# Kernel tuning notes

Measured on AMD Instinct MI355X. Metric: run time of the kernel, lower is better.

The kernel has to match this reference:

```python
import jax, jax.numpy as jnp
import numpy as np

DIM = 128
NUM_HEADS = 4
WS = 7          # window_size
SHIFT = 3       # shift_size
H = W = 56
B = 64
SCALE = DIM ** (-0.5)  # note: module scales by dim**-0.5, not head_dim**-0.5
NEG_INF = -1e9


def _make_attn_mask():
    # Static Swin shifted-window mask, built with numpy at trace time.
    img = np.zeros((H, W), dtype=np.float32)
    slices = (slice(0, -WS), slice(-WS, -SHIFT), slice(-SHIFT, None))
    cnt = 0
    for hs in slices:
        for ws_ in slices:
            img[hs, ws_] = cnt
            cnt += 1
    # window partition: [nW, WS*WS]
    m = img.reshape(H // WS, WS, W // WS, WS).transpose(0, 2, 1, 3).reshape(-1, WS * WS)
    am = m[:, None, :] - m[:, :, None]          # [nW, N, N]
    am = np.where(am != 0, NEG_INF, 0.0).astype(np.float32)
    return jnp.asarray(am)


def _window_partition(x):
    # x: [B, H, W, C] -> [B*nW, WS*WS, C]
    Bx, Hx, Wx, C = x.shape
    x = x.reshape(Bx, Hx // WS, WS, Wx // WS, WS, C)
    x = x.transpose(0, 1, 3, 2, 4, 5)
    return x.reshape(-1, WS * WS, C)


def _window_reverse(w):
    # w: [B*nW, WS*WS, C] -> [B, H, W, C]
    C = w.shape[-1]
    x = w.reshape(B, H // WS, W // WS, WS, WS, C)
    x = x.transpose(0, 1, 3, 2, 4, 5)
    return x.reshape(B, H, W, C)


def setup_inputs() -> dict:
    key = jax.random.key(0)
    k1, k2, k3 = jax.random.split(key, 3)
    x = jax.random.normal(k1, (B, H, W, DIM), dtype=jnp.float32)
    qkv_w = jax.random.normal(k2, (DIM, 3 * DIM), dtype=jnp.float32) * 0.02
    qkv_b = jnp.zeros((3 * DIM,), dtype=jnp.float32)
    proj_w = jax.random.normal(k3, (DIM, DIM), dtype=jnp.float32) * 0.02
    proj_b = jnp.zeros((DIM,), dtype=jnp.float32)
    return {"x": x, "qkv_w": qkv_w, "qkv_b": qkv_b, "proj_w": proj_w, "proj_b": proj_b}


def reference(x, qkv_w, qkv_b, proj_w, proj_b):
    attn_mask = _make_attn_mask()                       # [nW, N, N]
    N = WS * WS
    hd = DIM // NUM_HEADS

    shifted = jnp.roll(x, shift=(-SHIFT, -SHIFT), axis=(1, 2))
    xw = _window_partition(shifted)                     # [B*nW, N, C]

    qkv = xw @ qkv_w + qkv_b                            # [B*nW, N, 3C]
    qkv = qkv.reshape(-1, N, 3, NUM_HEADS, hd)
    q, k, v = qkv[:, :, 0], qkv[:, :, 1], qkv[:, :, 2]  # [B*nW, N, h, hd]

    attn = jnp.einsum('wnhd,wmhd->whnm', q, k) * SCALE  # [B*nW, h, N, N]
    nW = attn_mask.shape[0]
    attn = attn.reshape(B, nW, NUM_HEADS, N, N) + attn_mask[None, :, None, :, :]
    attn = jax.nn.softmax(attn.reshape(-1, NUM_HEADS, N, N), axis=-1)

    out = jnp.einsum('whnm,wmhd->wnhd', attn, v).reshape(-1, N, DIM)
    out = out @ proj_w + proj_b                         # [B*nW, N, C]

    shifted_out = _window_reverse(out)                  # [B, H, W, C]
    return jnp.roll(shifted_out, shift=(SHIFT, SHIFT), axis=(1, 2))
```

## Files before the change

### kernel.cpp

```cpp
#include <hip/hip_runtime.h>
#include <hip/hip_bf16.h>


#define NTOK 49
#define SCALE 0.08838834764831844f

typedef __bf16 bf16x8 __attribute__((ext_vector_type(8)));
typedef float  f32x4  __attribute__((ext_vector_type(4)));

__device__ __forceinline__ f32x4 mfma_bf16(bf16x8 a, bf16x8 b, f32x4 c) {
  return __builtin_amdgcn_mfma_f32_16x16x32_bf16(a, b, c, 0, 0, 0);
}

__device__ __forceinline__ ushort f2bf(float f) {
  __bf16 h = (__bf16)f;
  return __builtin_bit_cast(ushort, h);
}

__device__ __forceinline__ bf16x8 cvt8(f32x4 a, f32x4 b) {
  bf16x8 r;
#pragma unroll
  for (int j = 0; j < 4; ++j) { r[j] = (__bf16)a[j]; r[4 + j] = (__bf16)b[j]; }
  return r;
}

__device__ __forceinline__ int regid(int t, int wh, int ww) {
  int i = t / 7;
  int j = t - i * 7;
  int rh = (wh == 7) ? ((i < 4) ? 1 : 2) : 0;
  int rw = (ww == 7) ? ((j < 4) ? 1 : 2) : 0;
  return rh * 3 + rw;
}

__global__ void repack_w(const float* __restrict__ w, ushort* __restrict__ packed, int ncol) {
  int ctg  = blockIdx.x;
  int kt   = threadIdx.x >> 6;
  int lane = threadIdx.x & 63;
  int col  = ctg * 16 + (lane & 15);
  int k0   = kt * 32 + (lane >> 4) * 8;
  ushort* dst = packed + (size_t)((ctg * 4 + kt) * 64 + lane) * 8;
#pragma unroll
  for (int j = 0; j < 8; ++j) dst[j] = f2bf(w[(size_t)(k0 + j) * ncol + col]);
}

__global__ __launch_bounds__(256, 2)
void swin_fused(const float* __restrict__ x,
                const float* __restrict__ qkv_b,
                const float* __restrict__ proj_b,
                const ushort* __restrict__ pqkv,
                const ushort* __restrict__ pproj,
                float* __restrict__ out)
{
  __shared__ alignas(16) ushort lds[29696];

  const int wid = blockIdx.x;
  const int b   = wid >> 6;
  const int wh  = (wid >> 3) & 7;
  const int ww  = wid & 7;
  const int tid  = threadIdx.x;
  const int wave = tid >> 6;
  const int lane = tid & 63;
  const int lrow = lane & 15;
  const int lgrp = lane >> 4;

  ushort* const qb = lds + wave * 7424;
  ushort* const kb = qb + 2560;
  ushort* const vb = qb + 5120;
  ushort* const pb = qb;

  const f32x4 zf = {0.f, 0.f, 0.f, 0.f};

  bf16x8 a[4][4];
#pragma unroll
  for (int rt = 0; rt < 4; ++rt) {
    int token = rt * 16 + lrow;
    bool valid = token < NTOK;
    int tc = valid ? token : 0;
    int i = tc / 7;
    int j = tc - i * 7;
    int gh = wh * 7 + i + 3; if (gh >= 56) gh -= 56;
    int gw = ww * 7 + j + 3; if (gw >= 56) gw -= 56;
    const float* src = x + (((size_t)((b * 56 + gh) * 56 + gw)) << 7) + lgrp * 8;
#pragma unroll
    for (int kt = 0; kt < 4; ++kt) {
      f32x4 lo = *reinterpret_cast<const f32x4*>(src + kt * 32);
      f32x4 hi = *reinterpret_cast<const f32x4*>(src + kt * 32 + 4);
      bf16x8 v = cvt8(lo, hi);
      a[rt][kt] = valid ? v : bf16x8{};
    }
  }

#pragma unroll
  for (int o = 0; o < 3; ++o) {
    bf16x8 bw[2][4];
#pragma unroll
    for (int ct = 0; ct < 2; ++ct) {
      int ctg = o * 8 + wave * 2 + ct;
#pragma unroll
      for (int kt = 0; kt < 4; ++kt)
        bw[ct][kt] = *reinterpret_cast<const bf16x8*>(pqkv + (size_t)((ctg * 4 + kt) * 64 + lane) * 8);
    }
    f32x4 acc[4][2];
#pragma unroll
    for (int rt = 0; rt < 4; ++rt)
#pragma unroll
      for (int ct = 0; ct < 2; ++ct) {
        acc[rt][ct] = zf;
#pragma unroll
        for (int kt = 0; kt < 4; ++kt)
          acc[rt][ct] = mfma_bf16(a[rt][kt], bw[ct][kt], acc[rt][ct]);
      }
#pragma unroll
    for (int ct = 0; ct < 2; ++ct) {
      float bias = qkv_b[o * 128 + wave * 32 + ct * 16 + lrow];
#pragma unroll
      for (int rt = 0; rt < 4; ++rt)
#pragma unroll
        for (int r = 0; r < 4; ++r)
          acc[rt][ct][r] += bias;
    }
    if (o == 2) {
#pragma unroll
      for (int rt = 0; rt < 4; ++rt)
#pragma unroll
        for (int ct = 0; ct < 2; ++ct)
#pragma unroll
          for (int r = 0; r < 4; ++r) {
            int token = rt * 16 + lgrp * 4 + r;
            vb[(ct * 16 + lrow) * 72 + token] = f2bf(acc[rt][ct][r]);
          }
    } else {
      ushort* dst = (o == 0) ? qb : kb;
#pragma unroll
      for (int rt = 0; rt < 4; ++rt)
#pragma unroll
        for (int ct = 0; ct < 2; ++ct)
#pragma unroll
          for (int r = 0; r < 4; ++r) {
            int token = rt * 16 + lgrp * 4 + r;
            dst[token * 40 + ct * 16 + lrow] = f2bf(acc[rt][ct][r]);
          }
    }
  }

  bf16x8 aq[4], bk[4];
#pragma unroll
  for (int rt = 0; rt < 4; ++rt)
    aq[rt] = *reinterpret_cast<const bf16x8*>(qb + (rt * 16 + lrow) * 40 + lgrp * 8);
#pragma unroll
  for (int ct = 0; ct < 4; ++ct)
    bk[ct] = *reinterpret_cast<const bf16x8*>(kb + (ct * 16 + lrow) * 40 + lgrp * 8);

  f32x4 s[4][4];
#pragma unroll
  for (int rt = 0; rt < 4; ++rt)
#pragma unroll
    for (int ct = 0; ct < 4; ++ct)
      s[rt][ct] = mfma_bf16(aq[rt], bk[ct], zf);

  int cid[4]; bool cok[4];
#pragma unroll
  for (int ct = 0; ct < 4; ++ct) {
    int tc = ct * 16 + lrow;
    cok[ct] = tc < NTOK;
    cid[ct] = regid(tc, wh, ww);
  }

  float rinv[4][4];
#pragma unroll
  for (int rt = 0; rt < 4; ++rt) {
#pragma unroll
    for (int r = 0; r < 4; ++r) {
      int tr = rt * 16 + lgrp * 4 + r;
      int rid = regid(tr, wh, ww);
      float m = -3e38f;
#pragma unroll
      for (int ct = 0; ct < 4; ++ct) {
        float v = s[rt][ct][r] * SCALE;
        if (!cok[ct] || cid[ct] != rid) v = -1e9f;
        s[rt][ct][r] = v;
        m = fmaxf(m, v);
      }
      m = fmaxf(m, __shfl_xor(m, 1));
      m = fmaxf(m, __shfl_xor(m, 2));
      m = fmaxf(m, __shfl_xor(m, 4));
      m = fmaxf(m, __shfl_xor(m, 8));
      float sum = 0.f;
#pragma unroll
      for (int ct = 0; ct < 4; ++ct) {
        float e = __expf(s[rt][ct][r] - m);
        s[rt][ct][r] = e;
        sum += e;
      }
      sum += __shfl_xor(sum, 1);
      sum += __shfl_xor(sum, 2);
      sum += __shfl_xor(sum, 4);
      sum += __shfl_xor(sum, 8);
      rinv[rt][r] = 1.f / sum;
#pragma unroll
      for (int ct = 0; ct < 4; ++ct)
        pb[tr * 72 + ct * 16 + lrow] = f2bf(s[rt][ct][r]);
    }
  }

  bf16x8 ap[4][2], bv[2][2];
#pragma unroll
  for (int rt = 0; rt < 4; ++rt)
#pragma unroll
    for (int kt = 0; kt < 2; ++kt)
      ap[rt][kt] = *reinterpret_cast<const bf16x8*>(pb + (rt * 16 + lrow) * 72 + kt * 32 + lgrp * 8);
#pragma unroll
  for (int kt = 0; kt < 2; ++kt)
#pragma unroll
    for (int ct = 0; ct < 2; ++ct)
      bv[kt][ct] = *reinterpret_cast<const bf16x8*>(vb + (ct * 16 + lrow) * 72 + kt * 32 + lgrp * 8);

  f32x4 pv[4][2];
#pragma unroll
  for (int rt = 0; rt < 4; ++rt)
#pragma unroll
    for (int ct = 0; ct < 2; ++ct) {
      pv[rt][ct] = zf;
#pragma unroll
      for (int kt = 0; kt < 2; ++kt)
        pv[rt][ct] = mfma_bf16(ap[rt][kt], bv[kt][ct], pv[rt][ct]);
    }

  __syncthreads();

  ushort* const ao = lds;
#pragma unroll
  for (int rt = 0; rt < 4; ++rt)
#pragma unroll
    for (int ct = 0; ct < 2; ++ct)
#pragma unroll
      for (int r = 0; r < 4; ++r) {
        int token = rt * 16 + lgrp * 4 + r;
        ao[token * 136 + wave * 32 + ct * 16 + lrow] = f2bf(pv[rt][ct][r] * rinv[rt][r]);
      }
  __syncthreads();

  f32x4 acc2[4][2];
#pragma unroll
  for (int rt = 0; rt < 4; ++rt)
#pragma unroll
    for (int ct = 0; ct < 2; ++ct)
      acc2[rt][ct] = zf;
#pragma unroll
  for (int kt = 0; kt < 4; ++kt) {
    bf16x8 a2[4], b2[2];
#pragma unroll
    for (int rt = 0; rt < 4; ++rt)
      a2[rt] = *reinterpret_cast<const bf16x8*>(ao + (rt * 16 + lrow) * 136 + kt * 32 + lgrp * 8);
#pragma unroll
    for (int ct = 0; ct < 2; ++ct) {
      int ctg = wave * 2 + ct;
      b2[ct] = *reinterpret_cast<const bf16x8*>(pproj + (size_t)((ctg * 4 + kt) * 64 + lane) * 8);
    }
#pragma unroll
    for (int rt = 0; rt < 4; ++rt)
#pragma unroll
      for (int ct = 0; ct < 2; ++ct)
        acc2[rt][ct] = mfma_bf16(a2[rt], b2[ct], acc2[rt][ct]);
  }

  float bias2[2];
#pragma unroll
  for (int ct = 0; ct < 2; ++ct)
    bias2[ct] = proj_b[wave * 32 + ct * 16 + lrow];

#pragma unroll
  for (int rt = 0; rt < 4; ++rt)
#pragma unroll
    for (int r = 0; r < 4; ++r) {
      int token = rt * 16 + lgrp * 4 + r;
      if (token < NTOK) {
        int i = token / 7;
        int j = token - i * 7;
        int oh = wh * 7 + i + 3; if (oh >= 56) oh -= 56;
        int ow = ww * 7 + j + 3; if (ow >= 56) ow -= 56;
        float* dst = out + (((size_t)((b * 56 + oh) * 56 + ow)) << 7) + wave * 32;
#pragma unroll
        for (int ct = 0; ct < 2; ++ct)
          dst[ct * 16 + lrow] = acc2[rt][ct][r] + bias2[ct];
      }
    }
}

extern "C" void kernel_launch(void* const* d_in, const int* in_sizes, int n_in,
                              void* d_out, int out_size, void* d_ws, size_t ws_size,
                              hipStream_t stream) {
  const float* x      = (const float*)d_in[0];
  const float* qkv_w  = (const float*)d_in[1];
  const float* qkv_b  = (const float*)d_in[2];
  const float* proj_w = (const float*)d_in[3];
  const float* proj_b = (const float*)d_in[4];
  float* out = (float*)d_out;

  ushort* pqkv  = (ushort*)d_ws;
  ushort* pproj = pqkv + 49152;

  repack_w<<<24, 256, 0, stream>>>(qkv_w, pqkv, 384);
  repack_w<<<8, 256, 0, stream>>>(proj_w, pproj, 128);
  swin_fused<<<4096, 256, 0, stream>>>(x, qkv_b, proj_b, pqkv, pproj, out);
}
```

Baseline: 257.1 us.

## Keep attention operands in registers via ds_permute instead of LDS staging

Q, K, V and softmax probabilities now stay in registers. The transposed products (K·Q^T, W·X^T) are chosen so accumulator layouts line up, and ds_permute shuffles rebuild the MFMA input fragments, replacing the per-wave LDS staging buffers and their scattered 16-bit stores. The attention scale and log2(e) are folded into the packed Q weights and bias, so softmax uses exp2 and normalises the probabilities before the PV product. Shared memory shrinks to the projection staging buffer and launch bounds are raised to 3 blocks per SM, trading register pressure for occupancy and removing one barrier.

```diff
diff --git a/kernel.cpp b/kernel.cpp
--- a/kernel.cpp
+++ b/kernel.cpp
@@ -3,18 +3,20 @@
 
 
 #define NTOK 49
-#define SCALE 0.08838834764831844f
+#define QS (0.08838834764831844f * 1.4426950408889634f)
 
 typedef __bf16 bf16x8 __attribute__((ext_vector_type(8)));
+typedef __bf16 bf16x2 __attribute__((ext_vector_type(2)));
 typedef float  f32x4  __attribute__((ext_vector_type(4)));
+typedef unsigned int u32x4 __attribute__((ext_vector_type(4)));
 
 __device__ __forceinline__ f32x4 mfma_bf16(bf16x8 a, bf16x8 b, f32x4 c) {
   return __builtin_amdgcn_mfma_f32_16x16x32_bf16(a, b, c, 0, 0, 0);
 }
 
-__device__ __forceinline__ ushort f2bf(float f) {
-  __bf16 h = (__bf16)f;
-  return __builtin_bit_cast(ushort, h);
+__device__ __forceinline__ unsigned int pack2(float lo, float hi) {
+  bf16x2 t; t[0] = (__bf16)lo; t[1] = (__bf16)hi;
+  return __builtin_bit_cast(unsigned int, t);
 }
 
 __device__ __forceinline__ bf16x8 cvt8(f32x4 a, f32x4 b) {
@@ -22,6 +24,25 @@
 #pragma unroll
   for (int j = 0; j < 4; ++j) { r[j] = (__bf16)a[j]; r[4 + j] = (__bf16)b[j]; }
   return r;
+}
+
+__device__ __forceinline__ bf16x8 push_frag(unsigned int t0w0, unsigned int t0w1,
+                                            unsigned int t1w0, unsigned int t1w1,
+                                            int addrA, int addrB, int g0, int g1) {
+  unsigned int a0 = g0 ? t1w0 : t0w0;
+  unsigned int a1 = g0 ? t1w1 : t0w1;
+  unsigned int b0 = g0 ? t0w0 : t1w0;
+  unsigned int b1 = g0 ? t0w1 : t1w1;
+  unsigned int rA0 = (unsigned int)__builtin_amdgcn_ds_permute(addrA, (int)a0);
+  unsigned int rA1 = (unsigned int)__builtin_amdgcn_ds_permute(addrA, (int)a1);
+  unsigned int rB0 = (unsigned int)__builtin_amdgcn_ds_permute(addrB, (int)b0);
+  unsigned int rB1 = (unsigned int)__builtin_amdgcn_ds_permute(addrB, (int)b1);
+  u32x4 u;
+  u[0] = g1 ? rB0 : rA0;
+  u[1] = g1 ? rB1 : rA1;
+  u[2] = g1 ? rA0 : rB0;
+  u[3] = g1 ? rA1 : rB1;
+  return __builtin_bit_cast(bf16x8, u);
 }
 
 __device__ __forceinline__ int regid(int t, int wh, int ww) {
@@ -32,18 +53,23 @@
   return rh * 3 + rw;
 }
 
-__global__ void repack_w(const float* __restrict__ w, ushort* __restrict__ packed, int ncol) {
+__global__ void repack_w(const float* __restrict__ w, ushort* __restrict__ packed,
+                         int ncol, int scale_below, float scale) {
   int ctg  = blockIdx.x;
   int kt   = threadIdx.x >> 6;
   int lane = threadIdx.x & 63;
   int col  = ctg * 16 + (lane & 15);
   int k0   = kt * 32 + (lane >> 4) * 8;
+  float s  = (ctg < scale_below) ? scale : 1.0f;
   ushort* dst = packed + (size_t)((ctg * 4 + kt) * 64 + lane) * 8;
 #pragma unroll
-  for (int j = 0; j < 8; ++j) dst[j] = f2bf(w[(size_t)(k0 + j) * ncol + col]);
-}
-
-__global__ __launch_bounds__(256, 2)
+  for (int j = 0; j < 8; ++j) {
+    __bf16 h = (__bf16)(w[(size_t)(k0 + j) * ncol + col] * s);
+    dst[j] = __builtin_bit_cast(ushort, h);
+  }
+}
+
+__global__ __launch_bounds__(256, 3)
 void swin_fused(const float* __restrict__ x,
                 const float* __restrict__ qkv_b,
                 const float* __restrict__ proj_b,
@@ -51,7 +77,7 @@
                 const ushort* __restrict__ pproj,
                 float* __restrict__ out)
 {
-  __shared__ alignas(16) ushort lds[29696];
+  __shared__ alignas(16) ushort ao[64 * 136];
 
   const int wid = blockIdx.x;
   const int b   = wid >> 6;
@@ -60,229 +86,232 @@
   const int tid  = threadIdx.x;
   const int wave = tid >> 6;
   const int lane = tid & 63;
-  const int lrow = lane & 15;
-  const int lgrp = lane >> 4;
-
-  ushort* const qb = lds + wave * 7424;
-  ushort* const kb = qb + 2560;
-  ushort* const vb = qb + 5120;
-  ushort* const pb = qb;
-
+  const int c    = lane & 15;
+  const int g    = lane >> 4;
+  const int g0   = g & 1;
+  const int g1   = g >> 1;
+  const int addrA = (((2 * g0 + g1) << 4) | c) << 2;
+  const int addrB = (((2 * (1 - g0) + g1) << 4) | c) << 2;
   const f32x4 zf = {0.f, 0.f, 0.f, 0.f};
 
-  bf16x8 a[4][4];
-#pragma unroll
-  for (int rt = 0; rt < 4; ++rt) {
-    int token = rt * 16 + lrow;
+  bf16x8 xf[4][4];
+#pragma unroll
+  for (int nt = 0; nt < 4; ++nt) {
+    int token = nt * 16 + c;
     bool valid = token < NTOK;
     int tc = valid ? token : 0;
     int i = tc / 7;
     int j = tc - i * 7;
     int gh = wh * 7 + i + 3; if (gh >= 56) gh -= 56;
     int gw = ww * 7 + j + 3; if (gw >= 56) gw -= 56;
-    const float* src = x + (((size_t)((b * 56 + gh) * 56 + gw)) << 7) + lgrp * 8;
+    const float* src = x + (((size_t)((b * 56 + gh) * 56 + gw)) << 7) + g * 8;
 #pragma unroll
     for (int kt = 0; kt < 4; ++kt) {
       f32x4 lo = *reinterpret_cast<const f32x4*>(src + kt * 32);
       f32x4 hi = *reinterpret_cast<const f32x4*>(src + kt * 32 + 4);
       bf16x8 v = cvt8(lo, hi);
-      a[rt][kt] = valid ? v : bf16x8{};
-    }
-  }
-
-#pragma unroll
-  for (int o = 0; o < 3; ++o) {
-    bf16x8 bw[2][4];
-#pragma unroll
-    for (int ct = 0; ct < 2; ++ct) {
-      int ctg = o * 8 + wave * 2 + ct;
-#pragma unroll
-      for (int kt = 0; kt < 4; ++kt)
-        bw[ct][kt] = *reinterpret_cast<const bf16x8*>(pqkv + (size_t)((ctg * 4 + kt) * 64 + lane) * 8);
-    }
-    f32x4 acc[4][2];
-#pragma unroll
-    for (int rt = 0; rt < 4; ++rt)
-#pragma unroll
-      for (int ct = 0; ct < 2; ++ct) {
-        acc[rt][ct] = zf;
-#pragma unroll
-        for (int kt = 0; kt < 4; ++kt)
-          acc[rt][ct] = mfma_bf16(a[rt][kt], bw[ct][kt], acc[rt][ct]);
-      }
-#pragma unroll
-    for (int ct = 0; ct < 2; ++ct) {
-      float bias = qkv_b[o * 128 + wave * 32 + ct * 16 + lrow];
-#pragma unroll
-      for (int rt = 0; rt < 4; ++rt)
-#pragma unroll
-        for (int r = 0; r < 4; ++r)
-          acc[rt][ct][r] += bias;
-    }
-    if (o == 2) {
-#pragma unroll
-      for (int rt = 0; rt < 4; ++rt)
-#pragma unroll
-        for (int ct = 0; ct < 2; ++ct)
-#pragma unroll
-          for (int r = 0; r < 4; ++r) {
-            int token = rt * 16 + lgrp * 4 + r;
-            vb[(ct * 16 + lrow) * 72 + token] = f2bf(acc[rt][ct][r]);
-          }
-    } else {
-      ushort* dst = (o == 0) ? qb : kb;
-#pragma unroll
-      for (int rt = 0; rt < 4; ++rt)
-#pragma unroll
-        for (int ct = 0; ct < 2; ++ct)
-#pragma unroll
-          for (int r = 0; r < 4; ++r) {
-            int token = rt * 16 + lgrp * 4 + r;
-            dst[token * 40 + ct * 16 + lrow] = f2bf(acc[rt][ct][r]);
-          }
-    }
-  }
-
-  bf16x8 aq[4], bk[4];
-#pragma unroll
-  for (int rt = 0; rt < 4; ++rt)
-    aq[rt] = *reinterpret_cast<const bf16x8*>(qb + (rt * 16 + lrow) * 40 + lgrp * 8);
-#pragma unroll
-  for (int ct = 0; ct < 4; ++ct)
-    bk[ct] = *reinterpret_cast<const bf16x8*>(kb + (ct * 16 + lrow) * 40 + lgrp * 8);
-
-  f32x4 s[4][4];
-#pragma unroll
-  for (int rt = 0; rt < 4; ++rt)
-#pragma unroll
-    for (int ct = 0; ct < 4; ++ct)
-      s[rt][ct] = mfma_bf16(aq[rt], bk[ct], zf);
-
-  int cid[4]; bool cok[4];
-#pragma unroll
-  for (int ct = 0; ct < 4; ++ct) {
-    int tc = ct * 16 + lrow;
-    cok[ct] = tc < NTOK;
-    cid[ct] = regid(tc, wh, ww);
-  }
-
-  float rinv[4][4];
-#pragma unroll
-  for (int rt = 0; rt < 4; ++rt) {
+      xf[nt][kt] = valid ? v : bf16x8{};
+    }
+  }
+
+  unsigned int pkk[2][4][2], pkq[2][4][2], pkv[4][2][2];
+
+#pragma unroll
+  for (int o = 0; o < 2; ++o) {
+    f32x4 qc[2][4];
+#pragma unroll
+    for (int mt = 0; mt < 2; ++mt)
+#pragma unroll
+      for (int nt = 0; nt < 4; ++nt) qc[mt][nt] = zf;
+#pragma unroll
+    for (int kt = 0; kt < 4; ++kt) {
+      bf16x8 w0 = *reinterpret_cast<const bf16x8*>(
+          pqkv + (size_t)((((o ? 0 : 8) + wave * 2 + 0) * 4 + kt) * 64 + lane) * 8);
+      bf16x8 w1 = *reinterpret_cast<const bf16x8*>(
+          pqkv + (size_t)((((o ? 0 : 8) + wave * 2 + 1) * 4 + kt) * 64 + lane) * 8);
+#pragma unroll
+      for (int nt = 0; nt < 4; ++nt) {
+        qc[0][nt] = mfma_bf16(w0, xf[nt][kt], qc[0][nt]);
+        qc[1][nt] = mfma_bf16(w1, xf[nt][kt], qc[1][nt]);
+      }
+    }
+    float bscale = o ? QS : 1.0f;
+    int bbase = (o ? 0 : 128) + wave * 32;
+#pragma unroll
+    for (int mt = 0; mt < 2; ++mt)
+#pragma unroll
+      for (int r = 0; r < 4; ++r) {
+        float bv = qkv_b[bbase + mt * 16 + g * 4 + r] * bscale;
+#pragma unroll
+        for (int nt = 0; nt < 4; ++nt) qc[mt][nt][r] += bv;
+      }
+#pragma unroll
+    for (int mt = 0; mt < 2; ++mt)
+#pragma unroll
+      for (int nt = 0; nt < 4; ++nt) {
+        unsigned int* dst = o ? pkq[mt][nt] : pkk[mt][nt];
+        dst[0] = pack2(qc[mt][nt][0], qc[mt][nt][1]);
+        dst[1] = pack2(qc[mt][nt][2], qc[mt][nt][3]);
+      }
+  }
+
+  {
+    f32x4 vc[4][2];
+#pragma unroll
+    for (int mt = 0; mt < 4; ++mt) { vc[mt][0] = zf; vc[mt][1] = zf; }
+#pragma unroll
+    for (int kt = 0; kt < 4; ++kt) {
+      bf16x8 w0 = *reinterpret_cast<const bf16x8*>(
+          pqkv + (size_t)(((16 + wave * 2 + 0) * 4 + kt) * 64 + lane) * 8);
+      bf16x8 w1 = *reinterpret_cast<const bf16x8*>(
+          pqkv + (size_t)(((16 + wave * 2 + 1) * 4 + kt) * 64 + lane) * 8);
+#pragma unroll
+      for (int mt = 0; mt < 4; ++mt) {
+        vc[mt][0] = mfma_bf16(xf[mt][kt], w0, vc[mt][0]);
+        vc[mt][1] = mfma_bf16(xf[mt][kt], w1, vc[mt][1]);
+      }
+    }
+    float bv0 = qkv_b[256 + wave * 32 + c];
+    float bv1 = qkv_b[256 + wave * 32 + 16 + c];
+#pragma unroll
+    for (int mt = 0; mt < 4; ++mt)
+#pragma unroll
+      for (int r = 0; r < 4; ++r) { vc[mt][0][r] += bv0; vc[mt][1][r] += bv1; }
+#pragma unroll
+    for (int mt = 0; mt < 4; ++mt)
+#pragma unroll
+      for (int nv = 0; nv < 2; ++nv) {
+        pkv[mt][nv][0] = pack2(vc[mt][nv][0], vc[mt][nv][1]);
+        pkv[mt][nv][1] = pack2(vc[mt][nv][2], vc[mt][nv][3]);
+      }
+  }
+
+  bf16x8 ka[4], qa[4];
+#pragma unroll
+  for (int t4 = 0; t4 < 4; ++t4) {
+    ka[t4] = push_frag(pkk[0][t4][0], pkk[0][t4][1], pkk[1][t4][0], pkk[1][t4][1],
+                       addrA, addrB, g0, g1);
+    qa[t4] = push_frag(pkq[0][t4][0], pkq[0][t4][1], pkq[1][t4][0], pkq[1][t4][1],
+                       addrA, addrB, g0, g1);
+  }
+  f32x4 st[4][4];
+#pragma unroll
+  for (int m = 0; m < 4; ++m)
+#pragma unroll
+    for (int n = 0; n < 4; ++n)
+      st[m][n] = mfma_bf16(ka[m], qa[n], zf);
+
+  int ridq[4];
+#pragma unroll
+  for (int n = 0; n < 4; ++n) ridq[n] = regid(n * 16 + c, wh, ww);
+  int ridk[4][4];
+#pragma unroll
+  for (int m = 0; m < 4; ++m)
 #pragma unroll
     for (int r = 0; r < 4; ++r) {
-      int tr = rt * 16 + lgrp * 4 + r;
-      int rid = regid(tr, wh, ww);
-      float m = -3e38f;
-#pragma unroll
-      for (int ct = 0; ct < 4; ++ct) {
-        float v = s[rt][ct][r] * SCALE;
-        if (!cok[ct] || cid[ct] != rid) v = -1e9f;
-        s[rt][ct][r] = v;
-        m = fmaxf(m, v);
-      }
-      m = fmaxf(m, __shfl_xor(m, 1));
-      m = fmaxf(m, __shfl_xor(m, 2));
-      m = fmaxf(m, __shfl_xor(m, 4));
-      m = fmaxf(m, __shfl_xor(m, 8));
-      float sum = 0.f;
-#pragma unroll
-      for (int ct = 0; ct < 4; ++ct) {
-        float e = __expf(s[rt][ct][r] - m);
-        s[rt][ct][r] = e;
-        sum += e;
-      }
-      sum += __shfl_xor(sum, 1);
-      sum += __shfl_xor(sum, 2);
-      sum += __shfl_xor(sum, 4);
-      sum += __shfl_xor(sum, 8);
-      rinv[rt][r] = 1.f / sum;
-#pragma unroll
-      for (int ct = 0; ct < 4; ++ct)
-        pb[tr * 72 + ct * 16 + lrow] = f2bf(s[rt][ct][r]);
-    }
-  }
-
-  bf16x8 ap[4][2], bv[2][2];
-#pragma unroll
-  for (int rt = 0; rt < 4; ++rt)
-#pragma unroll
-    for (int kt = 0; kt < 2; ++kt)
-      ap[rt][kt] = *reinterpret_cast<const bf16x8*>(pb + (rt * 16 + lrow) * 72 + kt * 32 + lgrp * 8);
-#pragma unroll
-  for (int kt = 0; kt < 2; ++kt)
-#pragma unroll
-    for (int ct = 0; ct < 2; ++ct)
-      bv[kt][ct] = *reinterpret_cast<const bf16x8*>(vb + (ct * 16 + lrow) * 72 + kt * 32 + lgrp * 8);
-
-  f32x4 pv[4][2];
-#pragma unroll
-  for (int rt = 0; rt < 4; ++rt)
-#pragma unroll
-    for (int ct = 0; ct < 2; ++ct) {
-      pv[rt][ct] = zf;
-#pragma unroll
-      for (int kt = 0; kt < 2; ++kt)
-        pv[rt][ct] = mfma_bf16(ap[rt][kt], bv[kt][ct], pv[rt][ct]);
-    }
-
+      int kt_ = m * 16 + g * 4 + r;
+      ridk[m][r] = (kt_ < NTOK) ? regid(kt_, wh, ww) : -1;
+    }
+
+  unsigned int pkp[4][4][2];
+#pragma unroll
+  for (int n = 0; n < 4; ++n) {
+    float ev[4][4];
+    float mx = -1e30f;
+#pragma unroll
+    for (int m = 0; m < 4; ++m)
+#pragma unroll
+      for (int r = 0; r < 4; ++r) {
+        float v = (ridk[m][r] == ridq[n]) ? st[m][n][r] : -1e30f;
+        ev[m][r] = v;
+        mx = fmaxf(mx, v);
+      }
+    mx = fmaxf(mx, __shfl_xor(mx, 16));
+    mx = fmaxf(mx, __shfl_xor(mx, 32));
+    float sm = 0.f;
+#pragma unroll
+    for (int m = 0; m < 4; ++m)
+#pragma unroll
+      for (int r = 0; r < 4; ++r) {
+        float e = exp2f(ev[m][r] - mx);
+        ev[m][r] = e;
+        sm += e;
+      }
+    sm += __shfl_xor(sm, 16);
+    sm += __shfl_xor(sm, 32);
+    float rinv = __fdividef(1.f, sm);
+#pragma unroll
+    for (int m = 0; m < 4; ++m) {
+      pkp[m][n][0] = pack2(ev[m][0] * rinv, ev[m][1] * rinv);
+      pkp[m][n][1] = pack2(ev[m][2] * rinv, ev[m][3] * rinv);
+    }
+  }
+
+  f32x4 po[4][2];
+#pragma unroll
+  for (int m = 0; m < 4; ++m) { po[m][0] = zf; po[m][1] = zf; }
+#pragma unroll
+  for (int kt = 0; kt < 2; ++kt) {
+    bf16x8 vf0 = push_frag(pkv[2 * kt][0][0], pkv[2 * kt][0][1],
+                           pkv[2 * kt + 1][0][0], pkv[2 * kt + 1][0][1],
+                           addrA, addrB, g0, g1);
+    bf16x8 vf1 = push_frag(pkv[2 * kt][1][0], pkv[2 * kt][1][1],
+                           pkv[2 * kt + 1][1][0], pkv[2 * kt + 1][1][1],
+                           addrA, addrB, g0, g1);
+#pragma unroll
+    for (int m = 0; m < 4; ++m) {
+      bf16x8 pa = push_frag(pkp[2 * kt][m][0], pkp[2 * kt][m][1],
+                            pkp[2 * kt + 1][m][0], pkp[2 * kt + 1][m][1],
+                            addrA, addrB, g0, g1);
+      po[m][0] = mfma_bf16(pa, vf0, po[m][0]);
+      po[m][1] = mfma_bf16(pa, vf1, po[m][1]);
+    }
+  }
+
+#pragma unroll
+  for (int m = 0; m < 4; ++m)
+#pragma unroll
+    for (int nv = 0; nv < 2; ++nv)
+#pragma unroll
+      for (int r = 0; r < 4; ++r) {
+        __bf16 h = (__bf16)po[m][nv][r];
+        ao[(m * 16 + g * 4 + r) * 136 + wave * 32 + nv * 16 + c] =
+            __builtin_bit_cast(ushort, h);
+      }
   __syncthreads();
 
-  ushort* const ao = lds;
-#pragma unroll
-  for (int rt = 0; rt < 4; ++rt)
-#pragma unroll
-    for (int ct = 0; ct < 2; ++ct)
-#pragma unroll
-      for (int r = 0; r < 4; ++r) {
-        int token = rt * 16 + lgrp * 4 + r;
-        ao[token * 136 + wave * 32 + ct * 16 + lrow] = f2bf(pv[rt][ct][r] * rinv[rt][r]);
-      }
-  __syncthreads();
-
   f32x4 acc2[4][2];
 #pragma unroll
-  for (int rt = 0; rt < 4; ++rt)
-#pragma unroll
-    for (int ct = 0; ct < 2; ++ct)
-      acc2[rt][ct] = zf;
+  for (int m = 0; m < 4; ++m) { acc2[m][0] = zf; acc2[m][1] = zf; }
 #pragma unroll
   for (int kt = 0; kt < 4; ++kt) {
-    bf16x8 a2[4], b2[2];
-#pragma unroll
-    for (int rt = 0; rt < 4; ++rt)
-      a2[rt] = *reinterpret_cast<const bf16x8*>(ao + (rt * 16 + lrow) * 136 + kt * 32 + lgrp * 8);
-#pragma unroll
-    for (int ct = 0; ct < 2; ++ct) {
-      int ctg = wave * 2 + ct;
-      b2[ct] = *reinterpret_cast<const bf16x8*>(pproj + (size_t)((ctg * 4 + kt) * 64 + lane) * 8);
-    }
-#pragma unroll
-    for (int rt = 0; rt < 4; ++rt)
-#pragma unroll
-      for (int ct = 0; ct < 2; ++ct)
-        acc2[rt][ct] = mfma_bf16(a2[rt], b2[ct], acc2[rt][ct]);
-  }
-
-  float bias2[2];
-#pragma unroll
-  for (int ct = 0; ct < 2; ++ct)
-    bias2[ct] = proj_b[wave * 32 + ct * 16 + lrow];
-
-#pragma unroll
-  for (int rt = 0; rt < 4; ++rt)
+    bf16x8 b20 = *reinterpret_cast<const bf16x8*>(
+        pproj + (size_t)(((wave * 2 + 0) * 4 + kt) * 64 + lane) * 8);
+    bf16x8 b21 = *reinterpret_cast<const bf16x8*>(
+        pproj + (size_t)(((wave * 2 + 1) * 4 + kt) * 64 + lane) * 8);
+#pragma unroll
+    for (int m = 0; m < 4; ++m) {
+      bf16x8 af = *reinterpret_cast<const bf16x8*>(&ao[(m * 16 + c) * 136 + kt * 32 + g * 8]);
+      acc2[m][0] = mfma_bf16(af, b20, acc2[m][0]);
+      acc2[m][1] = mfma_bf16(af, b21, acc2[m][1]);
+    }
+  }
+  float pb0 = proj_b[wave * 32 + c];
+  float pb1 = proj_b[wave * 32 + 16 + c];
+
+#pragma unroll
+  for (int m = 0; m < 4; ++m)
 #pragma unroll
     for (int r = 0; r < 4; ++r) {
-      int token = rt * 16 + lgrp * 4 + r;
+      int token = m * 16 + g * 4 + r;
       if (token < NTOK) {
         int i = token / 7;
         int j = token - i * 7;
         int oh = wh * 7 + i + 3; if (oh >= 56) oh -= 56;
         int ow = ww * 7 + j + 3; if (ow >= 56) ow -= 56;
         float* dst = out + (((size_t)((b * 56 + oh) * 56 + ow)) << 7) + wave * 32;
-#pragma unroll
-        for (int ct = 0; ct < 2; ++ct)
-          dst[ct * 16 + lrow] = acc2[rt][ct][r] + bias2[ct];
+        dst[c]      = acc2[m][0][r] + pb0;
+        dst[16 + c] = acc2[m][1][r] + pb1;
       }
     }
 }
@@ -300,7 +329,7 @@
   ushort* pqkv  = (ushort*)d_ws;
   ushort* pproj = pqkv + 49152;
 
-  repack_w<<<24, 256, 0, stream>>>(qkv_w, pqkv, 384);
-  repack_w<<<8, 256, 0, stream>>>(proj_w, pproj, 128);
+  repack_w<<<24, 256, 0, stream>>>(qkv_w, pqkv, 384, 8, QS);
+  repack_w<<<8, 256, 0, stream>>>(proj_w, pproj, 128, 0, 1.0f);
   swin_fused<<<4096, 256, 0, stream>>>(x, qkv_b, proj_b, pqkv, pproj, out);
 }
```

New measurement: 259.1 us. Within noise of the previous version (+0.8%).
